# Kernel optimization log

Measured on AMD Instinct MI355X. Metric: run time of the kernel, lower is better.

Reference implementation:

```python
import jax, jax.numpy as jnp
import numpy as np

NEG_SLOPE = 0.2   # opt.alpha for LeakyReLU
NEG_INF = -9e15   # mask fill used by LocalAggregator

B, L, D, V = 512, 100, 128, 200000


def setup_inputs() -> dict:
    key = jax.random.key(0)
    ks = jax.random.split(key, 6)
    stdv = 1.0 / np.sqrt(D)
    inputs = jax.random.randint(ks[0], (B, L), 0, V)
    adj = jax.random.randint(ks[1], (B, L, L), 0, 5)        # edge types 0..4
    mask_item = jax.random.randint(ks[2], (B, L), 0, 2)
    item = jax.random.randint(ks[3], (B, L), 0, V)
    emb_table = jax.random.uniform(ks[4], (V, D), jnp.float32, -stdv, stdv)
    ka = jax.random.split(ks[5], 4)
    a0, a1, a2, a3 = [jax.random.uniform(k, (D,), jnp.float32, -stdv, stdv) for k in ka]
    return dict(inputs=inputs, adj=adj, mask_item=mask_item, item=item,
                emb_table=emb_table, a0=a0, a1=a1, a2=a2, a3=a3)


def reference(inputs, adj, mask_item, item, emb_table, a0, a1, a2, a3):
    # h = self.embedding(inputs)
    h = emb_table[inputs]  # [B, L, D]

    # LocalAggregator (GCE-GNN): a_input[b,i,j,:] = h[b,i,:] * h[b,j,:]
    # e_k = leakyrelu(a_input @ a_k); computed as a fused einsum (no BxLxLxD tensor)
    def att(a):
        return jax.nn.leaky_relu(jnp.einsum('bid,bjd,d->bij', h, h, a), NEG_SLOPE)

    e0, e1, e2, e3 = att(a0), att(a1), att(a2), att(a3)

    # select attention logit by edge type; non-edges masked to -9e15
    alpha = jnp.full_like(e0, NEG_INF)
    alpha = jnp.where(adj == 1, e0, alpha)
    alpha = jnp.where(adj == 2, e1, alpha)
    alpha = jnp.where(adj == 3, e2, alpha)
    alpha = jnp.where(adj == 4, e3, alpha)
    alpha = jax.nn.softmax(alpha, axis=-1)

    # output = alpha @ h (local aggregation); forward returns h_local
    return jnp.einsum('bij,bjd->bid', alpha, h)
```

## Files before the change

### kernel.cpp

```cpp
#include <hip/hip_runtime.h>
#include <hip/hip_bf16.h>

#define B_  512
#define L_  100
#define D_  128
#define SP_ 136
#define SO_ 132

typedef unsigned short ushort_t;
typedef __attribute__((ext_vector_type(8))) unsigned short us8;
typedef __attribute__((ext_vector_type(8))) __bf16 bf8;
typedef __attribute__((ext_vector_type(4))) float f4;
typedef __attribute__((ext_vector_type(4))) float f4v;
typedef __attribute__((ext_vector_type(4))) int i4v;
typedef __attribute__((ext_vector_type(4))) unsigned int ui4;

__device__ __forceinline__ float b2f(ushort_t u) {
  union { unsigned i; float f; } v; v.i = ((unsigned)u) << 16; return v.f;
}
__device__ __forceinline__ ushort_t f2b(float f) {
  unsigned u = __float_as_uint(f);
  u += 0x7fffu + ((u >> 16) & 1u);
  return (ushort_t)(u >> 16);
}
__device__ __forceinline__ us8 pack8(const float* x) {
  union { __hip_bfloat162 h; unsigned u; } cv;
  ui4 pk;
#pragma unroll
  for (int t = 0; t < 4; ++t) {
    cv.h = __float22bfloat162_rn(make_float2(x[2 * t], x[2 * t + 1]));
    pk[t] = cv.u;
  }
  return __builtin_bit_cast(us8, pk);
}
__device__ __forceinline__ int sw(int row, int col) {
  return row * 128 + ((((col >> 3) ^ row) & 15) << 3) + (col & 7);
}

__global__ __launch_bounds__(448, 4)
void CombineGraph_fused(const int* __restrict__ inp, const int* __restrict__ adjG,
                        const float* __restrict__ embF,
                        const float* __restrict__ a0F, const float* __restrict__ a1F,
                        const float* __restrict__ a2F, const float* __restrict__ a3F,
                        float* __restrict__ outG) {
  __shared__ __align__(16) unsigned char smem[75280];
  ushort_t* Hs = (ushort_t*)smem;
  ushort_t* Pt = (ushort_t*)(smem + 32768);
  unsigned char* adjS = smem + 63232;
  float* aVf = (float*)(smem + 73232);

  const int b = blockIdx.x, tid = threadIdx.x;
  const int w = tid / 64, lane = tid & 63, c = lane & 15, q = lane >> 4;

  for (int u = tid; u < 512; u += 448) {
    int k = u >> 7, d = u & 127;
    const float* ak = (k == 0) ? a0F : (k == 1) ? a1F : (k == 2) ? a2F : a3F;
    aVf[u] = ak[d];
  }
  for (int u = tid; u < 128 * 16; u += 448) {
    int r = u >> 4, ch = u & 15;
    us8 o = {0, 0, 0, 0, 0, 0, 0, 0};
    if (r < L_) {
      int idx = inp[b * L_ + r];
      const float* src = embF + ((size_t)idx << 7) + ch * 8;
      f4v v0 = *(const f4v*)src;
      f4v v1 = *(const f4v*)(src + 4);
      float x[8];
#pragma unroll
      for (int t = 0; t < 4; ++t) { x[t] = v0[t]; x[4 + t] = v1[t]; }
      o = pack8(x);
    }
    *(us8*)&Hs[sw(r, ch * 8)] = o;
  }
  for (int u = tid; u < 2500; u += 448) {
    i4v v = *(const i4v*)(adjG + (size_t)b * 10000 + u * 4);
    unsigned pk = (unsigned)(v[0] & 255) | ((unsigned)(v[1] & 255) << 8) |
                  ((unsigned)(v[2] & 255) << 16) | ((unsigned)(v[3] & 255) << 24);
    *(unsigned*)&adjS[u * 4] = pk;
  }
  __syncthreads();

  const int mi = w;

  unsigned tpk[7];
#pragma unroll
  for (int nt = 0; nt < 7; ++nt) {
    int j = nt * 16 + c;
    int jc = (j < L_) ? j : L_ - 1;
    unsigned pk = 0;
#pragma unroll
    for (int r = 0; r < 4; ++r) {
      int i = mi * 16 + q * 4 + r;
      int t = adjS[(i < L_ ? i : L_ - 1) * 100 + jc];
      t = (i < L_ && j < L_) ? t : 0;
      pk |= ((unsigned)t) << (8 * r);
    }
    tpk[nt] = pk;
  }

  float lg[7][4];
#pragma unroll
  for (int nt = 0; nt < 7; ++nt)
#pragma unroll
    for (int r = 0; r < 4; ++r) lg[nt][r] = -9e15f;

#pragma unroll
  for (int k = 0; k < 4; ++k) {
    us8 Afk[4];
#pragma unroll
    for (int ks = 0; ks < 4; ++ks) {
      us8 hr = *(const us8*)&Hs[sw(mi * 16 + c, ks * 32 + q * 8)];
      const float* ap = &aVf[k * 128 + ks * 32 + q * 8];
      f4v av0 = *(const f4v*)ap;
      f4v av1 = *(const f4v*)(ap + 4);
      float pr[8];
#pragma unroll
      for (int t = 0; t < 4; ++t) {
        pr[t]     = b2f(hr[t])     * av0[t];
        pr[4 + t] = b2f(hr[4 + t]) * av1[t];
      }
      Afk[ks] = pack8(pr);
    }
#pragma unroll
    for (int nt = 0; nt < 7; ++nt) {
      f4 acc = {0, 0, 0, 0};
#pragma unroll
      for (int ks = 0; ks < 4; ++ks) {
        bf8 bb = __builtin_bit_cast(bf8, *(const us8*)&Hs[sw(nt * 16 + c, ks * 32 + q * 8)]);
        acc = __builtin_amdgcn_mfma_f32_16x16x32_bf16(__builtin_bit_cast(bf8, Afk[ks]), bb, acc, 0, 0, 0);
      }
#pragma unroll
      for (int r = 0; r < 4; ++r) {
        int t = (int)((tpk[nt] >> (8 * r)) & 255u);
        float e = acc[r];
        e = (e > 0.f) ? e : 0.2f * e;
        lg[nt][r] = (t == k + 1) ? e : lg[nt][r];
      }
    }
    __builtin_amdgcn_sched_barrier(0);
  }

  ushort_t* Pw = Pt + w * 16 * SP_;
#pragma unroll
  for (int r = 0; r < 4; ++r) {
    float m = lg[0][r];
#pragma unroll
    for (int nt = 1; nt < 7; ++nt) m = fmaxf(m, lg[nt][r]);
#pragma unroll
    for (int off = 1; off <= 8; off <<= 1) m = fmaxf(m, __shfl_xor(m, off, 64));
    float ex[7], s = 0.f;
#pragma unroll
    for (int nt = 0; nt < 7; ++nt) { ex[nt] = __expf(lg[nt][r] - m); s += ex[nt]; }
#pragma unroll
    for (int off = 1; off <= 8; off <<= 1) s += __shfl_xor(s, off, 64);
    float inv = 1.0f / s;
    int row = q * 4 + r;
#pragma unroll
    for (int nt = 0; nt < 7; ++nt) Pw[row * SP_ + nt * 16 + c] = f2b(ex[nt] * inv);
  }
#pragma unroll
  for (int t = 0; t < 4; ++t) Pw[c * SP_ + 112 + q * 4 + t] = 0;

  __syncthreads();

  for (int u = tid; u < 8192; u += 448) {
    int d0 = u >> 7, j0 = u & 127;
    bool up = (j0 > d0);
    int d = up ? d0 : 127 - d0;
    int j = up ? j0 : 127 - j0;
    int ia = sw(d, j), ib = sw(j, d);
    ushort_t va = Hs[ia], vb = Hs[ib];
    Hs[ia] = vb; Hs[ib] = va;
  }
  __syncthreads();

  us8 Pf[4];
#pragma unroll
  for (int ks = 0; ks < 4; ++ks)
    Pf[ks] = *(const us8*)&Pw[c * SP_ + ks * 32 + q * 8];
  f4 oc[8];
#pragma unroll
  for (int nt2 = 0; nt2 < 8; ++nt2) {
    f4 a = {0, 0, 0, 0};
#pragma unroll
    for (int ks = 0; ks < 4; ++ks) {
      bf8 ob = __builtin_bit_cast(bf8, *(const us8*)&Hs[sw(nt2 * 16 + c, ks * 32 + q * 8)]);
      a = __builtin_amdgcn_mfma_f32_16x16x32_bf16(__builtin_bit_cast(bf8, Pf[ks]), ob, a, 0, 0, 0);
    }
    oc[nt2] = a;
  }
  __syncthreads();

  float* Ot = (float*)smem;
#pragma unroll
  for (int nt2 = 0; nt2 < 8; ++nt2)
#pragma unroll
    for (int r = 0; r < 4; ++r)
      Ot[(w * 16 + q * 4 + r) * SO_ + nt2 * 16 + c] = oc[nt2][r];
#pragma unroll
  for (int it = 0; it < 8; ++it) {
    int u = it * 64 + lane;
    int row16 = u >> 5, col4 = u & 31;
    int i = w * 16 + row16;
    if (i < L_) {
      f4 vv = *(const f4*)&Ot[(w * 16 + row16) * SO_ + col4 * 4];
      *(f4*)&outG[((size_t)b * L_ + i) * D_ + col4 * 4] = vv;
    }
  }
}

extern "C" void kernel_launch(void* const* d_in, const int* in_sizes, int n_in,
                              void* d_out, int out_size, void* d_ws, size_t ws_size,
                              hipStream_t stream) {
  (void)d_ws; (void)ws_size; (void)out_size;
  const int* inp = nullptr; const int* adj = nullptr;
  const float* emb = nullptr; const float* aP[4] = {nullptr, nullptr, nullptr, nullptr};
  int na = 0;
  for (int i = 0; i < n_in; ++i) {
    int s = in_sizes[i];
    if (s == 25600000)            emb = (const float*)d_in[i];
    else if (s == 5120000)        adj = (const int*)d_in[i];
    else if (s == 128 && na < 4)  aP[na++] = (const float*)d_in[i];
    else if (s == 51200 && !inp)  inp = (const int*)d_in[i];
  }
  CombineGraph_fused<<<dim3(B_), dim3(448), 0, stream>>>(
      inp, adj, emb, aP[0], aP[1], aP[2], aP[3], (float*)d_out);
}
```

Measured before the change: 190.8 us.

## Prefetch gathers into registers, read adjacency directly, pair attention MFMAs, split transpose

```diff
diff --git a/kernel.cpp b/kernel.cpp
--- a/kernel.cpp
+++ b/kernel.cpp
@@ -12,7 +12,6 @@
 typedef __attribute__((ext_vector_type(8))) __bf16 bf8;
 typedef __attribute__((ext_vector_type(4))) float f4;
 typedef __attribute__((ext_vector_type(4))) float f4v;
-typedef __attribute__((ext_vector_type(4))) int i4v;
 typedef __attribute__((ext_vector_type(4))) unsigned int ui4;
 
 __device__ __forceinline__ float b2f(ushort_t u) {
@@ -43,57 +42,81 @@
                         const float* __restrict__ a0F, const float* __restrict__ a1F,
                         const float* __restrict__ a2F, const float* __restrict__ a3F,
                         float* __restrict__ outG) {
-  __shared__ __align__(16) unsigned char smem[75280];
+  __shared__ __align__(16) unsigned char smem[65280];
   ushort_t* Hs = (ushort_t*)smem;
   ushort_t* Pt = (ushort_t*)(smem + 32768);
-  unsigned char* adjS = smem + 63232;
-  float* aVf = (float*)(smem + 73232);
+  float* aVf = (float*)(smem + 63232);
 
   const int b = blockIdx.x, tid = threadIdx.x;
   const int w = tid / 64, lane = tid & 63, c = lane & 15, q = lane >> 4;
+  const int mi = w;
+
+  int idxv[5];
+#pragma unroll
+  for (int it = 0; it < 5; ++it) {
+    int u = tid + it * 448;
+    int r = u >> 4;
+    idxv[it] = (u < 2048 && r < L_) ? inp[b * L_ + r] : 0;
+  }
+
+  f4v ev0[5], ev1[5];
+#pragma unroll
+  for (int it = 0; it < 5; ++it) {
+    int u = tid + it * 448;
+    int r = u >> 4, ch = u & 15;
+    if (u < 2048 && r < L_) {
+      const float* src = embF + ((size_t)idxv[it] << 7) + ch * 8;
+      ev0[it] = *(const f4v*)src;
+      ev1[it] = *(const f4v*)(src + 4);
+    }
+  }
+
+  int tv[7][4];
+#pragma unroll
+  for (int nt = 0; nt < 7; ++nt) {
+    int j = nt * 16 + c;
+    int jc = (j < L_) ? j : L_ - 1;
+#pragma unroll
+    for (int r4 = 0; r4 < 4; ++r4) {
+      int i = mi * 16 + q * 4 + r4;
+      int ic = (i < L_) ? i : L_ - 1;
+      tv[nt][r4] = adjG[(size_t)b * 10000 + ic * 100 + jc];
+    }
+  }
 
   for (int u = tid; u < 512; u += 448) {
     int k = u >> 7, d = u & 127;
     const float* ak = (k == 0) ? a0F : (k == 1) ? a1F : (k == 2) ? a2F : a3F;
     aVf[u] = ak[d];
   }
-  for (int u = tid; u < 128 * 16; u += 448) {
-    int r = u >> 4, ch = u & 15;
-    us8 o = {0, 0, 0, 0, 0, 0, 0, 0};
-    if (r < L_) {
-      int idx = inp[b * L_ + r];
-      const float* src = embF + ((size_t)idx << 7) + ch * 8;
-      f4v v0 = *(const f4v*)src;
-      f4v v1 = *(const f4v*)(src + 4);
-      float x[8];
-#pragma unroll
-      for (int t = 0; t < 4; ++t) { x[t] = v0[t]; x[4 + t] = v1[t]; }
-      o = pack8(x);
-    }
-    *(us8*)&Hs[sw(r, ch * 8)] = o;
-  }
-  for (int u = tid; u < 2500; u += 448) {
-    i4v v = *(const i4v*)(adjG + (size_t)b * 10000 + u * 4);
-    unsigned pk = (unsigned)(v[0] & 255) | ((unsigned)(v[1] & 255) << 8) |
-                  ((unsigned)(v[2] & 255) << 16) | ((unsigned)(v[3] & 255) << 24);
-    *(unsigned*)&adjS[u * 4] = pk;
-  }
-  __syncthreads();
-
-  const int mi = w;
+
+#pragma unroll
+  for (int it = 0; it < 5; ++it) {
+    int u = tid + it * 448;
+    if (u < 2048) {
+      int r = u >> 4, ch = u & 15;
+      us8 o = {0, 0, 0, 0, 0, 0, 0, 0};
+      if (r < L_) {
+        float x[8];
+#pragma unroll
+        for (int t = 0; t < 4; ++t) { x[t] = ev0[it][t]; x[4 + t] = ev1[it][t]; }
+        o = pack8(x);
+      }
+      *(us8*)&Hs[sw(r, ch * 8)] = o;
+    }
+  }
+  __syncthreads();
 
   unsigned tpk[7];
 #pragma unroll
   for (int nt = 0; nt < 7; ++nt) {
     int j = nt * 16 + c;
-    int jc = (j < L_) ? j : L_ - 1;
     unsigned pk = 0;
 #pragma unroll
-    for (int r = 0; r < 4; ++r) {
-      int i = mi * 16 + q * 4 + r;
-      int t = adjS[(i < L_ ? i : L_ - 1) * 100 + jc];
-      t = (i < L_ && j < L_) ? t : 0;
-      pk |= ((unsigned)t) << (8 * r);
+    for (int r4 = 0; r4 < 4; ++r4) {
+      int i = mi * 16 + q * 4 + r4;
+      int t = (i < L_ && j < L_) ? tv[nt][r4] : 0;
+      pk |= ((unsigned)t) << (8 * r4);
     }
     tpk[nt] = pk;
   }
@@ -102,82 +125,108 @@
 #pragma unroll
   for (int nt = 0; nt < 7; ++nt)
 #pragma unroll
-    for (int r = 0; r < 4; ++r) lg[nt][r] = -9e15f;
-
-#pragma unroll
-  for (int k = 0; k < 4; ++k) {
-    us8 Afk[4];
+    for (int r4 = 0; r4 < 4; ++r4) lg[nt][r4] = -9e15f;
+
+#pragma unroll
+  for (int p = 0; p < 2; ++p) {
+    us8 Af2[2][4];
 #pragma unroll
     for (int ks = 0; ks < 4; ++ks) {
       us8 hr = *(const us8*)&Hs[sw(mi * 16 + c, ks * 32 + q * 8)];
-      const float* ap = &aVf[k * 128 + ks * 32 + q * 8];
-      f4v av0 = *(const f4v*)ap;
-      f4v av1 = *(const f4v*)(ap + 4);
-      float pr[8];
-#pragma unroll
-      for (int t = 0; t < 4; ++t) {
-        pr[t]     = b2f(hr[t])     * av0[t];
-        pr[4 + t] = b2f(hr[4 + t]) * av1[t];
-      }
-      Afk[ks] = pack8(pr);
+      float hfv[8];
+#pragma unroll
+      for (int jj = 0; jj < 8; ++jj) hfv[jj] = b2f(hr[jj]);
+#pragma unroll
+      for (int kk = 0; kk < 2; ++kk) {
+        const float* ap = &aVf[(p * 2 + kk) * 128 + ks * 32 + q * 8];
+        f4v av0 = *(const f4v*)ap;
+        f4v av1 = *(const f4v*)(ap + 4);
+        float pr[8];
+#pragma unroll
+        for (int t = 0; t < 4; ++t) {
+          pr[t]     = hfv[t]     * av0[t];
+          pr[4 + t] = hfv[4 + t] * av1[t];
+        }
+        Af2[kk][ks] = pack8(pr);
+      }
     }
 #pragma unroll
     for (int nt = 0; nt < 7; ++nt) {
-      f4 acc = {0, 0, 0, 0};
+      f4 ac0 = {0, 0, 0, 0}, ac1 = {0, 0, 0, 0};
 #pragma unroll
       for (int ks = 0; ks < 4; ++ks) {
         bf8 bb = __builtin_bit_cast(bf8, *(const us8*)&Hs[sw(nt * 16 + c, ks * 32 + q * 8)]);
-        acc = __builtin_amdgcn_mfma_f32_16x16x32_bf16(__builtin_bit_cast(bf8, Afk[ks]), bb, acc, 0, 0, 0);
-      }
-#pragma unroll
-      for (int r = 0; r < 4; ++r) {
-        int t = (int)((tpk[nt] >> (8 * r)) & 255u);
-        float e = acc[r];
-        e = (e > 0.f) ? e : 0.2f * e;
-        lg[nt][r] = (t == k + 1) ? e : lg[nt][r];
+        ac0 = __builtin_amdgcn_mfma_f32_16x16x32_bf16(__builtin_bit_cast(bf8, Af2[0][ks]), bb, ac0, 0, 0, 0);
+        ac1 = __builtin_amdgcn_mfma_f32_16x16x32_bf16(__builtin_bit_cast(bf8, Af2[1][ks]), bb, ac1, 0, 0, 0);
+      }
+#pragma unroll
+      for (int r4 = 0; r4 < 4; ++r4) {
+        int t = (int)((tpk[nt] >> (8 * r4)) & 255u);
+        float e0 = ac0[r4]; e0 = (e0 > 0.f) ? e0 : 0.2f * e0;
+        float e1 = ac1[r4]; e1 = (e1 > 0.f) ? e1 : 0.2f * e1;
+        lg[nt][r4] = (t == 2 * p + 1) ? e0 : lg[nt][r4];
+        lg[nt][r4] = (t == 2 * p + 2) ? e1 : lg[nt][r4];
       }
     }
     __builtin_amdgcn_sched_barrier(0);
   }
 
+  unsigned vt[19];
+#pragma unroll
+  for (int it = 0; it < 19; ++it) {
+    int u = tid + it * 448;
+    if (u < 8192) {
+      int d0 = u >> 7, j0 = u & 127;
+      bool up = (j0 > d0);
+      int d = up ? d0 : 127 - d0;
+      int j = up ? j0 : 127 - j0;
+      unsigned va = Hs[sw(d, j)], vb = Hs[sw(j, d)];
+      vt[it] = va | (vb << 16);
+    }
+  }
+
   ushort_t* Pw = Pt + w * 16 * SP_;
 #pragma unroll
-  for (int r = 0; r < 4; ++r) {
-    float m = lg[0][r];
-#pragma unroll
-    for (int nt = 1; nt < 7; ++nt) m = fmaxf(m, lg[nt][r]);
+  for (int r4 = 0; r4 < 4; ++r4) {
+    float m = lg[0][r4];
+#pragma unroll
+    for (int nt = 1; nt < 7; ++nt) m = fmaxf(m, lg[nt][r4]);
 #pragma unroll
     for (int off = 1; off <= 8; off <<= 1) m = fmaxf(m, __shfl_xor(m, off, 64));
     float ex[7], s = 0.f;
 #pragma unroll
-    for (int nt = 0; nt < 7; ++nt) { ex[nt] = __expf(lg[nt][r] - m); s += ex[nt]; }
+    for (int nt = 0; nt < 7; ++nt) { ex[nt] = __expf(lg[nt][r4] - m); s += ex[nt]; }
 #pragma unroll
     for (int off = 1; off <= 8; off <<= 1) s += __shfl_xor(s, off, 64);
     float inv = 1.0f / s;
-    int row = q * 4 + r;
+    int row = q * 4 + r4;
 #pragma unroll
     for (int nt = 0; nt < 7; ++nt) Pw[row * SP_ + nt * 16 + c] = f2b(ex[nt] * inv);
   }
 #pragma unroll
   for (int t = 0; t < 4; ++t) Pw[c * SP_ + 112 + q * 4 + t] = 0;
 
-  __syncthreads();
-
-  for (int u = tid; u < 8192; u += 448) {
-    int d0 = u >> 7, j0 = u & 127;
-    bool up = (j0 > d0);
-    int d = up ? d0 : 127 - d0;
-    int j = up ? j0 : 127 - j0;
-    int ia = sw(d, j), ib = sw(j, d);
-    ushort_t va = Hs[ia], vb = Hs[ib];
-    Hs[ia] = vb; Hs[ib] = va;
-  }
   __syncthreads();
 
   us8 Pf[4];
 #pragma unroll
   for (int ks = 0; ks < 4; ++ks)
     Pf[ks] = *(const us8*)&Pw[c * SP_ + ks * 32 + q * 8];
+
+#pragma unroll
+  for (int it = 0; it < 19; ++it) {
+    int u = tid + it * 448;
+    if (u < 8192) {
+      int d0 = u >> 7, j0 = u & 127;
+      bool up = (j0 > d0);
+      int d = up ? d0 : 127 - d0;
+      int j = up ? j0 : 127 - j0;
+      Hs[sw(d, j)] = (ushort_t)(vt[it] >> 16);
+      Hs[sw(j, d)] = (ushort_t)(vt[it] & 0xffffu);
+    }
+  }
+  __syncthreads();
+
   f4 oc[8];
 #pragma unroll
   for (int nt2 = 0; nt2 < 8; ++nt2) {
@@ -195,8 +244,8 @@
 #pragma unroll
   for (int nt2 = 0; nt2 < 8; ++nt2)
 #pragma unroll
-    for (int r = 0; r < 4; ++r)
-      Ot[(w * 16 + q * 4 + r) * SO_ + nt2 * 16 + c] = oc[nt2][r];
+    for (int r4 = 0; r4 < 4; ++r4)
+      Ot[(w * 16 + q * 4 + r4) * SO_ + nt2 * 16 + c] = oc[nt2][r4];
 #pragma unroll
   for (int it = 0; it < 8; ++it) {
     int u = it * 64 + lane;
```

After: 216.1 us. 1.13x slower.
